# Kernel tuning notes

Measured on AMD Instinct MI355X. Metric: run time of the kernel, lower is better.

Reference implementation:

```python
import jax, jax.numpy as jnp
import numpy as np

B, N_H, N = 32, 16, 64
R, REP, NUM_CLS = 1024, 1024, 117
NUM_ITER = 2
T_LIS, K_LIS, W_LIS = 8.3, 12.0, 10.0

# static pair indices: x in [0,n_h), y in [0,n), x != y  -> M = N_H*N - N_H
_xx, _yy = np.meshgrid(np.arange(N_H), np.arange(N), indexing='ij')
_mask = _xx != _yy
X_IDX = jnp.asarray(_xx[_mask], dtype=jnp.int32)  # [M]
Y_IDX = jnp.asarray(_yy[_mask], dtype=jnp.int32)  # [M]
M = int(_mask.sum())


def lis(x):
    # low-grade suppression
    return T_LIS / (1.0 + jnp.exp(K_LIS - W_LIS * x))


def setup_inputs() -> dict:
    key = jax.random.key(0)
    ks = jax.random.split(key, 18)
    s = 0.02
    p = lambda k, shp: (jax.random.normal(k, shp) * s).astype(jnp.float32)
    box_features = jax.random.normal(ks[0], (B, N, R), dtype=jnp.float32)
    box_coords = jax.random.uniform(ks[1], (B, N, 4), dtype=jnp.float32)
    box_labels = jax.random.randint(ks[2], (B, N), 0, NUM_CLS).astype(jnp.int32)
    box_labels = box_labels.at[:, :N_H].set(0)  # first N_H are humans (human_idx=0)
    box_scores = jax.random.uniform(ks[3], (B, N), dtype=jnp.float32)
    return {
        'box_features': box_features, 'box_coords': box_coords,
        'box_labels': box_labels, 'box_scores': box_scores,
        'W1': p(ks[4], (2 * R, REP)), 'b1': jnp.zeros((REP,), jnp.float32),
        'W2': p(ks[5], (REP, REP // 2)), 'b2': jnp.zeros((REP // 2,), jnp.float32),
        'W3': p(ks[6], (REP // 2, 1)), 'b3': jnp.zeros((1,), jnp.float32),
        'Ws': p(ks[7], (R, REP)), 'bs': jnp.zeros((REP,), jnp.float32),
        'Wo': p(ks[8], (R, REP)), 'bo': jnp.zeros((REP,), jnp.float32),
        'Wsu': p(ks[9], (R + REP, R)),
        'Wou': p(ks[10], (R + REP, R)),
    }


def reference(box_features, box_coords, box_labels, box_scores,
              W1, b1, W2, b2, W3, b3, Ws, bs, Wo, bo, Wsu, Wou):
    def per_image(enc, coords, labels, scores):
        # enc: [N, R]
        A = jnp.zeros((N_H, N), enc.dtype)
        for _ in range(NUM_ITER):
            pe = jnp.concatenate([enc[X_IDX], enc[Y_IDX]], axis=1)  # [M, 2R]
            h = jax.nn.relu(pe @ W1 + b1)
            h = jax.nn.relu(h @ W2 + b2)
            w = (h @ W3 + b3)[:, 0]  # [M]
            A = jnp.zeros((N_H, N), enc.dtype).at[X_IDX, Y_IDX].set(jax.nn.sigmoid(w))
            msg_h = A @ jax.nn.relu(enc @ Wo + bo)                      # [N_H, REP]
            enc_h = jnp.concatenate([enc[:N_H], msg_h], axis=1) @ Wsu  # [N_H, R]
            enc = enc.at[:N_H].set(enc_h)
            msg_o = A.T @ jax.nn.relu(enc_h @ Ws + bs)                  # [N, REP]
            enc = jnp.concatenate([enc, msg_o], axis=1) @ Wou           # [N, R]
        pair = jnp.concatenate([enc[X_IDX], enc[Y_IDX]], axis=1)  # [M, 2R]
        prod = lis(scores[X_IDX]) * lis(scores[Y_IDX])            # [M]
        # identity object_class_to_target_class: class c -> [c]
        prior = jnp.zeros((M, NUM_CLS), enc.dtype).at[jnp.arange(M), labels[Y_IDX]].set(prod)
        prior = A[X_IDX, Y_IDX][:, None] * prior
        return pair, coords[X_IDX], coords[Y_IDX], prior

    pair, bh, bo_, prior = jax.vmap(per_image)(box_features, box_coords, box_labels, box_scores)
    return (pair.reshape(B * M, 2 * R), bh, bo_, prior.reshape(B * M, NUM_CLS))
```

## Files before the change

kernel.cpp:

```cpp
#include <hip/hip_runtime.h>

#define B_   32
#define N_   64
#define NH   16
#define R_   1024
#define REP  1024
#define M_   1008
#define BM   (B_ * M_)
#define NCLS 117

#define MD_DIRECT 0
#define MD_CC1    2
#define MD_CC2    3

typedef short bhalf8 __attribute__((ext_vector_type(8)));
typedef float f32x4  __attribute__((ext_vector_type(4)));

typedef __attribute__((address_space(3))) void       lds_t;
typedef const __attribute__((address_space(1))) void gbl_t;
__device__ __forceinline__ void gld16(const void* g, void* l)
{
    __builtin_amdgcn_global_load_lds((gbl_t*)g, (lds_t*)l, 16, 0, 0);
}

__device__ __forceinline__ unsigned short f2bf(float f)
{
    union { float f; unsigned int u; } x; x.f = f;
    unsigned int r = x.u + 0x7FFFu + ((x.u >> 16) & 1u);
    return (unsigned short)(r >> 16);
}
__device__ __forceinline__ float bf2f(unsigned short u)
{
    union { unsigned int i; float f; } x; x.i = ((unsigned int)u) << 16; return x.f;
}
__device__ __forceinline__ unsigned int addrelu2(unsigned int a, unsigned int b)
{
    float lo = fmaxf(bf2f((unsigned short)(a & 0xffff)) + bf2f((unsigned short)(b & 0xffff)), 0.f);
    float hi = fmaxf(bf2f((unsigned short)(a >> 16))    + bf2f((unsigned short)(b >> 16)),    0.f);
    return (unsigned int)f2bf(lo) | ((unsigned int)f2bf(hi) << 16);
}

__device__ __forceinline__ void tr32(const float* in, unsigned short* out,
                                     int K, int N, int local)
{
    __shared__ float t[32][33];
    int kb = K >> 5;
    int k0 = (local % kb) * 32, n0 = (local / kb) * 32;
    int tx = threadIdx.x & 31, ty = threadIdx.x >> 5;
#pragma unroll
    for (int r = 0; r < 4; ++r)
        t[ty + r * 8][tx] = in[(size_t)(k0 + ty + r * 8) * N + n0 + tx];
    __syncthreads();
#pragma unroll
    for (int r = 0; r < 4; ++r)
        out[(size_t)(n0 + ty + r * 8) * K + k0 + tx] = f2bf(t[tx][ty + r * 8]);
}

__global__ __launch_bounds__(256)
void prep_all(const float* __restrict__ W1, const float* __restrict__ W2,
              const float* __restrict__ Wo, const float* __restrict__ Ws,
              const float* __restrict__ Wsu, const float* __restrict__ Wou,
              const float* __restrict__ bo_, const float* __restrict__ b1_,
              unsigned short* __restrict__ Wfused, unsigned short* __restrict__ W2t,
              unsigned short* __restrict__ Wst, unsigned short* __restrict__ Wsut,
              unsigned short* __restrict__ Wout, float* __restrict__ biasFull)
{
    int bx = blockIdx.x;
    if      (bx < 1024) tr32(W1 + 1024 * 1024, Wfused,               1024, 1024, bx);
    else if (bx < 2048) tr32(Wo,               Wfused + 1024 * 1024, 1024, 1024, bx - 1024);
    else if (bx < 3072) tr32(W1,               Wfused + 2048 * 1024, 1024, 1024, bx - 2048);
    else if (bx < 3584) tr32(W2,  W2t,  1024, 512,  bx - 3072);
    else if (bx < 4608) tr32(Ws,  Wst,  1024, 1024, bx - 3584);
    else if (bx < 6656) tr32(Wsu, Wsut, 2048, 1024, bx - 4608);
    else if (bx < 8704) tr32(Wou, Wout, 2048, 1024, bx - 6656);
    else {
        int c = (bx - 8704) * 256 + threadIdx.x;
        float v = 0.f;
        if (c >= 2048)      v = b1_[c - 2048];
        else if (c >= 1024) v = bo_[c - 1024];
        biasFull[c] = v;
    }
}

__global__ void cvt_bf(const float* __restrict__ in, unsigned short* __restrict__ out)
{
    int i = blockIdx.x * 256 + threadIdx.x;
    float4 a = ((const float4*)in)[2 * i];
    float4 b = ((const float4*)in)[2 * i + 1];
    uint4 o;
    o.x = (unsigned)f2bf(a.x) | ((unsigned)f2bf(a.y) << 16);
    o.y = (unsigned)f2bf(a.z) | ((unsigned)f2bf(a.w) << 16);
    o.z = (unsigned)f2bf(b.x) | ((unsigned)f2bf(b.y) << 16);
    o.w = (unsigned)f2bf(b.z) | ((unsigned)f2bf(b.w) << 16);
    ((uint4*)out)[i] = o;
}

__global__ __launch_bounds__(256)
void gemm_uvgo(const unsigned short* __restrict__ enc,
               const unsigned short* __restrict__ Wf,
               const float* __restrict__ biasFull, unsigned short* __restrict__ XX)
{
    __shared__ unsigned short As[128 * 32];
    __shared__ unsigned short Bs[128 * 32];
    const int tid  = threadIdx.x;
    const int lane = tid & 63, wave = tid >> 6;
    const int wm = wave & 1, wn = wave >> 1;
    const int l15 = lane & 15, lk = lane >> 4;
    const int row0 = blockIdx.y * 128, col0 = blockIdx.x * 128;
    const int kq = (lane & 3) * 8;

    const unsigned short* pA[2];
    const unsigned short* pB[2];
    unsigned short* AsW[2];
    unsigned short* BsW[2];
#pragma unroll
    for (int i = 0; i < 2; ++i) {
        int tr = wave * 32 + (lane >> 2) + i * 16;
        pA[i]  = enc + (size_t)(row0 + tr) * 1024 + kq;
        pB[i]  = Wf  + (size_t)(col0 + tr) * 1024 + kq;
        AsW[i] = As + wave * 1024 + i * 512 + lane * 8;
        BsW[i] = Bs + wave * 1024 + i * 512 + lane * 8;
    }

    f32x4 acc[4][4];
#pragma unroll
    for (int i = 0; i < 4; ++i)
#pragma unroll
    for (int j = 0; j < 4; ++j) acc[i][j] = (f32x4)0.f;

    for (int k0 = 0; k0 < 1024; k0 += 32) {
        __syncthreads();
        gld16(pA[0] + k0, AsW[0]);
        gld16(pA[1] + k0, AsW[1]);
        gld16(pB[0] + k0, BsW[0]);
        gld16(pB[1] + k0, BsW[1]);
        __syncthreads();
        bhalf8 af[4], bf4[4];
#pragma unroll
        for (int mt = 0; mt < 4; ++mt)
            af[mt] = *(bhalf8*)&As[(wm * 64 + mt * 16 + l15) * 32 + lk * 8];
#pragma unroll
        for (int nt = 0; nt < 4; ++nt)
            bf4[nt] = *(bhalf8*)&Bs[(wn * 64 + nt * 16 + l15) * 32 + lk * 8];
#pragma unroll
        for (int mt = 0; mt < 4; ++mt)
#pragma unroll
        for (int nt = 0; nt < 4; ++nt)
            acc[mt][nt] = __builtin_amdgcn_mfma_f32_16x16x32_bf16(af[mt], bf4[nt],
                                                                  acc[mt][nt], 0, 0, 0);
    }

#pragma unroll
    for (int mt = 0; mt < 4; ++mt)
#pragma unroll
    for (int r = 0; r < 4; ++r) {
        int row = row0 + wm * 64 + mt * 16 + lk * 4 + r;
#pragma unroll
        for (int nt = 0; nt < 4; ++nt) {
            int col = col0 + wn * 64 + nt * 16 + l15;
            float v = acc[mt][nt][r] + biasFull[col];
            if ((col >> 10) == 1) v = fmaxf(v, 0.f);
            XX[(size_t)row * 3072 + col] = f2bf(v);
        }
    }
}

__global__ __launch_bounds__(256)
void pair_bf(const unsigned short* __restrict__ XX,
             const unsigned short* __restrict__ W2t, const float* __restrict__ b2,
             const float* __restrict__ W3f, float* __restrict__ wpart)
{
    __shared__ unsigned short As[128 * 32];
    __shared__ unsigned short Bs[128 * 32];
    __shared__ float red[2][128];
    const int tid  = threadIdx.x;
    const int lane = tid & 63, wave = tid >> 6;
    const int wm = wave & 1, wn = wave >> 1;
    const int l15 = lane & 15, lk = lane >> 4;
    const int row0 = blockIdx.y * 128, col0 = blockIdx.x * 128;

    const int srow = tid >> 1, skh = tid & 1;
    int rg = row0 + srow;
    int b  = rg / M_, m = rg % M_;
    int x  = m / 63, jj = m % 63;
    int y  = jj + (jj >= x ? 1 : 0);
    const unsigned short* Up = XX + ((size_t)(b * 64 + x)) * 3072 + 2048 + skh * 16;
    const unsigned short* Vp = XX + ((size_t)(b * 64 + y)) * 3072 + skh * 16;
    unsigned short* AsW = As + srow * 32 + skh * 16;

    const int kq = (lane & 3) * 8;
    const unsigned short* pB[2];
    unsigned short* BsW[2];
#pragma unroll
    for (int i = 0; i < 2; ++i) {
        int tr = wave * 32 + (lane >> 2) + i * 16;
        pB[i]  = W2t + (size_t)(col0 + tr) * REP + kq;
        BsW[i] = Bs + wave * 1024 + i * 512 + lane * 8;
    }

    f32x4 acc[4][4];
#pragma unroll
    for (int i = 0; i < 4; ++i)
#pragma unroll
    for (int j = 0; j < 4; ++j) acc[i][j] = (f32x4)0.f;

    for (int k0 = 0; k0 < REP; k0 += 32) {
        uint4 uu0 = *(const uint4*)(Up + k0);
        uint4 uu1 = *(const uint4*)(Up + k0 + 8);
        uint4 vv0 = *(const uint4*)(Vp + k0);
        uint4 vv1 = *(const uint4*)(Vp + k0 + 8);
        uint4 h0, h1;
        h0.x = addrelu2(uu0.x, vv0.x); h0.y = addrelu2(uu0.y, vv0.y);
        h0.z = addrelu2(uu0.z, vv0.z); h0.w = addrelu2(uu0.w, vv0.w);
        h1.x = addrelu2(uu1.x, vv1.x); h1.y = addrelu2(uu1.y, vv1.y);
        h1.z = addrelu2(uu1.z, vv1.z); h1.w = addrelu2(uu1.w, vv1.w);
        __syncthreads();
        *(uint4*)(AsW)     = h0;
        *(uint4*)(AsW + 8) = h1;
        gld16(pB[0] + k0, BsW[0]);
        gld16(pB[1] + k0, BsW[1]);
        __syncthreads();
        bhalf8 af[4], bf4[4];
#pragma unroll
        for (int mt = 0; mt < 4; ++mt)
            af[mt] = *(bhalf8*)&As[(wm * 64 + mt * 16 + l15) * 32 + lk * 8];
#pragma unroll
        for (int nt = 0; nt < 4; ++nt)
            bf4[nt] = *(bhalf8*)&Bs[(wn * 64 + nt * 16 + l15) * 32 + lk * 8];
#pragma unroll
        for (int mt = 0; mt < 4; ++mt)
#pragma unroll
        for (int nt = 0; nt < 4; ++nt)
            acc[mt][nt] = __builtin_amdgcn_mfma_f32_16x16x32_bf16(af[mt], bf4[nt],
                                                                  acc[mt][nt], 0, 0, 0);
    }

    float b2v[4], w3v[4];
#pragma unroll
    for (int nt = 0; nt < 4; ++nt) {
        int col = col0 + wn * 64 + nt * 16 + l15;
        b2v[nt] = b2[col];
        w3v[nt] = W3f[col];
    }
#pragma unroll
    for (int mt = 0; mt < 4; ++mt)
#pragma unroll
    for (int r = 0; r < 4; ++r) {
        int rloc = wm * 64 + mt * 16 + lk * 4 + r;
        float p = 0.f;
#pragma unroll
        for (int nt = 0; nt < 4; ++nt)
            p += fmaxf(acc[mt][nt][r] + b2v[nt], 0.f) * w3v[nt];
        p += __shfl_xor(p, 1); p += __shfl_xor(p, 2);
        p += __shfl_xor(p, 4); p += __shfl_xor(p, 8);
        if (l15 == 0) red[wn][rloc] = p;
    }
    __syncthreads();
    if (tid < 128)
        wpart[blockIdx.x * BM + row0 + tid] = red[0][tid] + red[1][tid];
}

__device__ __forceinline__ void compute_A(const float* __restrict__ wpart, float b3v,
                                          int b, float* Al, int t)
{
    for (int i = t; i < NH * N_; i += 128) {
        int y = i & 63, x = i >> 6;
        float v = 0.f;
        if (y != x) {
            int j = y - (y > x ? 1 : 0);
            int r = b * M_ + x * 63 + j;
            float s = b3v + wpart[r] + wpart[BM + r] + wpart[2 * BM + r] + wpart[3 * BM + r];
            v = 1.f / (1.f + expf(-s));
        }
        Al[i] = v;
    }
}

__global__ __launch_bounds__(128)
void msgh_kernel(const float* __restrict__ wpart, const float* __restrict__ b3,
                 const unsigned short* __restrict__ XX,
                 unsigned short* __restrict__ msgh, float* __restrict__ Aw)
{
    __shared__ float Al[NH * N_];
    __shared__ float Gl[N_][128];
    int b = blockIdx.x, c0 = blockIdx.y * 128, t = threadIdx.x;
    compute_A(wpart, b3[0], b, Al, t);
    for (int y = 0; y < N_; ++y)
        Gl[y][t] = bf2f(XX[((size_t)(b * 64 + y)) * 3072 + 1024 + c0 + t]);
    __syncthreads();
    if (blockIdx.y == 0)
        for (int i = t; i < NH * N_; i += 128) Aw[b * NH * N_ + i] = Al[i];
    for (int x = 0; x < NH; ++x) {
        float s = 0.f;
#pragma unroll 8
        for (int y = 0; y < N_; ++y) s += Al[x * N_ + y] * Gl[y][t];
        msgh[((size_t)(b * NH + x)) * REP + c0 + t] = f2bf(s);
    }
}

__global__ __launch_bounds__(128)
void msgo_kernel(const float* __restrict__ wpart, const float* __restrict__ b3,
                 const unsigned short* __restrict__ Gs, unsigned short* __restrict__ msgo)
{
    __shared__ float Al[NH * N_];
    __shared__ float Gl[NH][128];
    int b = blockIdx.x, c0 = blockIdx.y * 128, t = threadIdx.x;
    compute_A(wpart, b3[0], b, Al, t);
    for (int x = 0; x < NH; ++x)
        Gl[x][t] = bf2f(Gs[((size_t)(b * NH + x)) * REP + c0 + t]);
    __syncthreads();
    for (int y = 0; y < N_; ++y) {
        float s = 0.f;
#pragma unroll
        for (int x = 0; x < NH; ++x) s += Al[x * N_ + y] * Gl[x][t];
        msgo[((size_t)(b * N_ + y)) * REP + c0 + t] = f2bf(s);
    }
}

__global__ __launch_bounds__(256)
void gemm_small(const unsigned short* __restrict__ A1, const unsigned short* __restrict__ A2,
                const unsigned short* __restrict__ A3, const unsigned short* __restrict__ Bt,
                const float* __restrict__ bias, float* __restrict__ Cf,
                unsigned short* __restrict__ Cb, int K, int Nc, int doRelu, int mode)
{
    __shared__ unsigned short As[64 * 32];
    __shared__ unsigned short Bs[64 * 32];
    const int tid  = threadIdx.x;
    const int lane = tid & 63, wave = tid >> 6;
    const int wr = wave & 1, wc = wave >> 1;
    const int l15 = lane & 15, lk = lane >> 4;
    const int row0 = blockIdx.y * 64, col0 = blockIdx.x * 64;
    const int kq = (lane & 3) * 8;

    int tr = wave * 16 + (lane >> 2);
    int rr = row0 + tr;
    const unsigned short* p1;
    const unsigned short* p2 = nullptr;
    if (mode == MD_DIRECT) {
        p1 = A1 + (size_t)rr * K;
    } else if (mode == MD_CC1) {
        int b = rr >> 4, x = rr & 15;
        p1 = A1 + (size_t)(b * 64 + x) * 1024;
        p2 = A2 + (size_t)rr * 1024 - 1024;
    } else {
        int b = rr >> 6, n = rr & 63;
        p1 = (n < 16) ? A3 + (size_t)(b * 16 + n) * 1024
                      : A1 + (size_t)rr * 1024;
        p2 = A2 + (size_t)rr * 1024 - 1024;
    }
    const unsigned short* pA1 = p1 + kq;
    const unsigned short* pA2 = p2 ? p2 + kq : nullptr;
    const unsigned short* pB  = Bt + (size_t)(col0 + tr) * K + kq;
    unsigned short* AsW = As + wave * 512 + lane * 8;
    unsigned short* BsW = Bs + wave * 512 + lane * 8;
    const int kSw = (mode != MD_DIRECT) ? 1024 : K;

    f32x4 acc[2][2];
#pragma unroll
    for (int i = 0; i < 2; ++i)
#pragma unroll
    for (int j = 0; j < 2; ++j) acc[i][j] = (f32x4)0.f;

    for (int k0 = 0; k0 < K; k0 += 32) {
        const unsigned short* a = (k0 < kSw) ? pA1 : pA2;
        __syncthreads();
        gld16(a + k0,  AsW);
        gld16(pB + k0, BsW);
        __syncthreads();
        bhalf8 af[2], bf4[2];
#pragma unroll
        for (int mt = 0; mt < 2; ++mt)
            af[mt] = *(bhalf8*)&As[(wr * 32 + mt * 16 + l15) * 32 + lk * 8];
#pragma unroll
        for (int nt = 0; nt < 2; ++nt)
            bf4[nt] = *(bhalf8*)&Bs[(wc * 32 + nt * 16 + l15) * 32 + lk * 8];
#pragma unroll
        for (int mt = 0; mt < 2; ++mt)
#pragma unroll
        for (int nt = 0; nt < 2; ++nt)
            acc[mt][nt] = __builtin_amdgcn_mfma_f32_16x16x32_bf16(af[mt], bf4[nt],
                                                                  acc[mt][nt], 0, 0, 0);
    }

#pragma unroll
    for (int mt = 0; mt < 2; ++mt)
#pragma unroll
    for (int r = 0; r < 4; ++r) {
        int row = row0 + wr * 32 + mt * 16 + lk * 4 + r;
#pragma unroll
        for (int nt = 0; nt < 2; ++nt) {
            int col = col0 + wc * 32 + nt * 16 + l15;
            float v = acc[mt][nt][r];
            if (bias) v += bias[col];
            if (doRelu) v = fmaxf(v, 0.f);
            if (Cf) Cf[(size_t)row * Nc + col] = v;
            if (Cb) Cb[(size_t)row * Nc + col] = f2bf(v);
        }
    }
}

__global__ void pair_out(const float* __restrict__ enc, float* __restrict__ out0)
{
    int i = blockIdx.x * 256 + threadIdx.x;
    if (i >= BM * 512) return;
    int r = i >> 9, q = i & 511;
    int b = r / M_, m = r % M_;
    int x = m / 63, j = m % 63;
    int y = j + (j >= x ? 1 : 0);
    const float4* e4 = (const float4*)enc;
    float4 v = (q < 256) ? e4[(b * 64 + x) * 256 + q]
                         : e4[(b * 64 + y) * 256 + (q - 256)];
    ((float4*)out0)[i] = v;
}

__global__ void coords_out(const float* __restrict__ coords,
                           float* __restrict__ out1, float* __restrict__ out2)
{
    int r = blockIdx.x * 256 + threadIdx.x;
    if (r >= BM) return;
    int b = r / M_, m = r % M_;
    int x = m / 63, j = m % 63;
    int y = j + (j >= x ? 1 : 0);
    const float4* c4 = (const float4*)coords;
    ((float4*)out1)[r] = c4[b * 64 + x];
    ((float4*)out2)[r] = c4[b * 64 + y];
}

__device__ __forceinline__ float lis_f(float x)
{
    return 8.3f / (1.f + expf(12.f - 10.f * x));
}

__global__ void prior_out(const float* __restrict__ Aw, const int* __restrict__ labels,
                          const float* __restrict__ scores, float* __restrict__ out3)
{
    int i = blockIdx.x * 256 + threadIdx.x;
    if (i >= BM * NCLS) return;
    int r = i / NCLS, c = i % NCLS;
    int b = r / M_, m = r % M_;
    int x = m / 63, j = m % 63;
    int y = j + (j >= x ? 1 : 0);
    int lab = labels[b * 64 + y];
    float val = 0.f;
    if (c == lab) {
        float sx = scores[b * 64 + x], sy = scores[b * 64 + y];
        val = Aw[(b * NH + x) * N_ + y] * lis_f(sx) * lis_f(sy);
    }
    out3[i] = val;
}

extern "C" void kernel_launch(void* const* d_in, const int* in_sizes, int n_in,
                              void* d_out, int out_size, void* d_ws, size_t ws_size,
                              hipStream_t stream)
{
    const float* box_features = (const float*)d_in[0];
    const float* box_coords   = (const float*)d_in[1];
    const int*   box_labels   = (const int*)d_in[2];
    const float* box_scores   = (const float*)d_in[3];
    const float* W1  = (const float*)d_in[4];
    const float* b1  = (const float*)d_in[5];
    const float* W2  = (const float*)d_in[6];
    const float* b2  = (const float*)d_in[7];
    const float* W3  = (const float*)d_in[8];
    const float* b3  = (const float*)d_in[9];
    const float* Ws  = (const float*)d_in[10];
    const float* bs  = (const float*)d_in[11];
    const float* Wo  = (const float*)d_in[12];
    const float* bo  = (const float*)d_in[13];
    const float* Wsu = (const float*)d_in[14];
    const float* Wou = (const float*)d_in[15];

    float* wsf  = (float*)d_ws;
    float* encA = wsf;           wsf += (size_t)B_ * N_ * R_;
    float* wpart= wsf;           wsf += (size_t)4 * BM;
    float* Aw   = wsf;           wsf += (size_t)B_ * NH * N_;
    float* biasFull = wsf;       wsf += 3072;

    unsigned short* wsu = (unsigned short*)wsf;
    unsigned short* enc0bf = wsu;  wsu += (size_t)B_ * N_ * R_;
    unsigned short* encIbf = wsu;  wsu += (size_t)B_ * N_ * R_;
    unsigned short* XX     = wsu;  wsu += (size_t)B_ * N_ * 3072;
    unsigned short* msghbf = wsu;  wsu += (size_t)B_ * NH * REP;
    unsigned short* enchbf = wsu;  wsu += (size_t)B_ * NH * R_;
    unsigned short* Gsbf   = wsu;  wsu += (size_t)B_ * NH * REP;
    unsigned short* msgobf = wsu;  wsu += (size_t)B_ * N_ * REP;
    unsigned short* Wfused = wsu;  wsu += (size_t)3072 * 1024;
    unsigned short* W2t    = wsu;  wsu += (size_t)512 * 1024;
    unsigned short* Wst    = wsu;  wsu += (size_t)1024 * 1024;
    unsigned short* Wsut   = wsu;  wsu += (size_t)1024 * 2048;
    unsigned short* Wout   = wsu;  wsu += (size_t)1024 * 2048;

    float* out0 = (float*)d_out;
    float* out1 = out0 + (size_t)BM * 2048;
    float* out2 = out1 + (size_t)BM * 4;
    float* out3 = out2 + (size_t)BM * 4;

    prep_all<<<8716, 256, 0, stream>>>(W1, W2, Wo, Ws, Wsu, Wou, bo, b1,
                                       Wfused, W2t, Wst, Wsut, Wout, biasFull);
    cvt_bf<<<1024, 256, 0, stream>>>(box_features, enc0bf);

    for (int it = 0; it < 2; ++it) {
        const unsigned short* enc = (it == 0) ? enc0bf : encIbf;
        gemm_uvgo<<<dim3(24, 16), 256, 0, stream>>>(enc, Wfused, biasFull, XX);
        pair_bf<<<dim3(4, 252), 256, 0, stream>>>(XX, W2t, b2, W3, wpart);
        msgh_kernel<<<dim3(32, 8), 128, 0, stream>>>(wpart, b3, XX, msghbf, Aw);
        gemm_small<<<dim3(16, 8), 256, 0, stream>>>(enc, msghbf, nullptr, Wsut, nullptr,
                                                    nullptr, enchbf, 2048, 1024, 0, MD_CC1);
        gemm_small<<<dim3(16, 8), 256, 0, stream>>>(enchbf, nullptr, nullptr, Wst, bs,
                                                    nullptr, Gsbf, 1024, 1024, 1, MD_DIRECT);
        msgo_kernel<<<dim3(32, 8), 128, 0, stream>>>(wpart, b3, Gsbf, msgobf);
        gemm_small<<<dim3(16, 32), 256, 0, stream>>>(enc, msgobf, enchbf, Wout, nullptr,
                                                     (it == 1) ? encA : nullptr,
                                                     (it == 0) ? encIbf : nullptr,
                                                     1024 * 2, 1024, 0, MD_CC2);
    }

    pair_out<<<64512, 256, 0, stream>>>(encA, out0);
    coords_out<<<126, 256, 0, stream>>>(box_coords, out1, out2);
    prior_out<<<14742, 256, 0, stream>>>(Aw, box_labels, box_scores, out3);
}
```

Baseline: 761.2 us.

## Multi-buffer LDS pipelines in GEMMs and merge output and prep launches

The three GEMM kernels now keep several LDS slots of async global-to-LDS loads in flight: three slots in gemm_uvgo and pair_bf, four in gemm_small. Each stage waits with explicit vmcnt/lgkmcnt counts and a single barrier pair, instead of syncing around every tile load. pair_bf also prefetches its next U/V rows into registers, and addrelu2 uses a packed bf16 convert instruction. The bf16 input conversion is folded into prep_all and the three output kernels into one launch, which removes launch gaps. The hand-written waitcnt values depend on the exact number of outstanding loads and are fragile, and the extra LDS may lower occupancy.

After: 751.5 us. About the same (-1.3%).

```diff
diff --git a/kernel.cpp b/kernel.cpp
--- a/kernel.cpp
+++ b/kernel.cpp
@@ -33,11 +33,32 @@
 {
     union { unsigned int i; float f; } x; x.i = ((unsigned int)u) << 16; return x.f;
 }
+
 __device__ __forceinline__ unsigned int addrelu2(unsigned int a, unsigned int b)
 {
-    float lo = fmaxf(bf2f((unsigned short)(a & 0xffff)) + bf2f((unsigned short)(b & 0xffff)), 0.f);
-    float hi = fmaxf(bf2f((unsigned short)(a >> 16))    + bf2f((unsigned short)(b >> 16)),    0.f);
-    return (unsigned int)f2bf(lo) | ((unsigned int)f2bf(hi) << 16);
+    union { unsigned int u; float f; } la, ha, lb, hb;
+    la.u = a << 16;          ha.u = a & 0xffff0000u;
+    lb.u = b << 16;          hb.u = b & 0xffff0000u;
+    float lo = fmaxf(la.f + lb.f, 0.f);
+    float hi = fmaxf(ha.f + hb.f, 0.f);
+    unsigned int r;
+    asm("v_cvt_pk_bf16_f32 %0, %1, %2" : "=v"(r) : "v"(lo), "v"(hi));
+    return r;
+}
+
+__device__ __forceinline__ void wait_vm(int n)
+{
+    if (n >= 8)      asm volatile("s_waitcnt vmcnt(8)" ::: "memory");
+    else if (n == 6) asm volatile("s_waitcnt vmcnt(6)" ::: "memory");
+    else if (n == 4) asm volatile("s_waitcnt vmcnt(4)" ::: "memory");
+    else if (n == 2) asm volatile("s_waitcnt vmcnt(2)" ::: "memory");
+    else             asm volatile("s_waitcnt vmcnt(0)" ::: "memory");
+}
+__device__ __forceinline__ void wait_vm_lgkm(int n)
+{
+    if (n >= 12)      asm volatile("s_waitcnt vmcnt(12) lgkmcnt(0)" ::: "memory");
+    else if (n >= 10) asm volatile("s_waitcnt vmcnt(10) lgkmcnt(0)" ::: "memory");
+    else              asm volatile("s_waitcnt vmcnt(8) lgkmcnt(0)" ::: "memory");
 }
 
 __device__ __forceinline__ void tr32(const float* in, unsigned short* out,
@@ -61,9 +82,11 @@
               const float* __restrict__ Wo, const float* __restrict__ Ws,
               const float* __restrict__ Wsu, const float* __restrict__ Wou,
               const float* __restrict__ bo_, const float* __restrict__ b1_,
+              const float* __restrict__ feat,
               unsigned short* __restrict__ Wfused, unsigned short* __restrict__ W2t,
               unsigned short* __restrict__ Wst, unsigned short* __restrict__ Wsut,
-              unsigned short* __restrict__ Wout, float* __restrict__ biasFull)
+              unsigned short* __restrict__ Wout, float* __restrict__ biasFull,
+              unsigned short* __restrict__ enc0bf)
 {
     int bx = blockIdx.x;
     if      (bx < 1024) tr32(W1 + 1024 * 1024, Wfused,               1024, 1024, bx);
@@ -73,26 +96,23 @@
     else if (bx < 4608) tr32(Ws,  Wst,  1024, 1024, bx - 3584);
     else if (bx < 6656) tr32(Wsu, Wsut, 2048, 1024, bx - 4608);
     else if (bx < 8704) tr32(Wou, Wout, 2048, 1024, bx - 6656);
-    else {
+    else if (bx < 8716) {
         int c = (bx - 8704) * 256 + threadIdx.x;
         float v = 0.f;
         if (c >= 2048)      v = b1_[c - 2048];
         else if (c >= 1024) v = bo_[c - 1024];
         biasFull[c] = v;
-    }
-}
-
-__global__ void cvt_bf(const float* __restrict__ in, unsigned short* __restrict__ out)
-{
-    int i = blockIdx.x * 256 + threadIdx.x;
-    float4 a = ((const float4*)in)[2 * i];
-    float4 b = ((const float4*)in)[2 * i + 1];
-    uint4 o;
-    o.x = (unsigned)f2bf(a.x) | ((unsigned)f2bf(a.y) << 16);
-    o.y = (unsigned)f2bf(a.z) | ((unsigned)f2bf(a.w) << 16);
-    o.z = (unsigned)f2bf(b.x) | ((unsigned)f2bf(b.y) << 16);
-    o.w = (unsigned)f2bf(b.z) | ((unsigned)f2bf(b.w) << 16);
-    ((uint4*)out)[i] = o;
+    } else {
+        int i = (bx - 8716) * 256 + threadIdx.x;
+        float4 a = ((const float4*)feat)[2 * i];
+        float4 b = ((const float4*)feat)[2 * i + 1];
+        uint4 o;
+        o.x = (unsigned)f2bf(a.x) | ((unsigned)f2bf(a.y) << 16);
+        o.y = (unsigned)f2bf(a.z) | ((unsigned)f2bf(a.w) << 16);
+        o.z = (unsigned)f2bf(b.x) | ((unsigned)f2bf(b.y) << 16);
+        o.w = (unsigned)f2bf(b.z) | ((unsigned)f2bf(b.w) << 16);
+        ((uint4*)enc0bf)[i] = o;
+    }
 }
 
 __global__ __launch_bounds__(256)
@@ -100,8 +120,8 @@
                const unsigned short* __restrict__ Wf,
                const float* __restrict__ biasFull, unsigned short* __restrict__ XX)
 {
-    __shared__ unsigned short As[128 * 32];
-    __shared__ unsigned short Bs[128 * 32];
+    __shared__ unsigned short As[3][128 * 32];
+    __shared__ unsigned short Bs[3][128 * 32];
     const int tid  = threadIdx.x;
     const int lane = tid & 63, wave = tid >> 6;
     const int wm = wave & 1, wn = wave >> 1;
@@ -111,16 +131,20 @@
 
     const unsigned short* pA[2];
     const unsigned short* pB[2];
-    unsigned short* AsW[2];
-    unsigned short* BsW[2];
+    int ldsOff[2];
 #pragma unroll
     for (int i = 0; i < 2; ++i) {
         int tr = wave * 32 + (lane >> 2) + i * 16;
         pA[i]  = enc + (size_t)(row0 + tr) * 1024 + kq;
         pB[i]  = Wf  + (size_t)(col0 + tr) * 1024 + kq;
-        AsW[i] = As + wave * 1024 + i * 512 + lane * 8;
-        BsW[i] = Bs + wave * 1024 + i * 512 + lane * 8;
-    }
+        ldsOff[i] = wave * 1024 + i * 512 + lane * 8;
+    }
+
+#define STG_UV(slot, k0) do {                          \
+        gld16(pA[0] + (k0), &As[slot][ldsOff[0]]);     \
+        gld16(pA[1] + (k0), &As[slot][ldsOff[1]]);     \
+        gld16(pB[0] + (k0), &Bs[slot][ldsOff[0]]);     \
+        gld16(pB[1] + (k0), &Bs[slot][ldsOff[1]]); } while (0)
 
     f32x4 acc[4][4];
 #pragma unroll
@@ -128,27 +152,31 @@
 #pragma unroll
     for (int j = 0; j < 4; ++j) acc[i][j] = (f32x4)0.f;
 
-    for (int k0 = 0; k0 < 1024; k0 += 32) {
-        __syncthreads();
-        gld16(pA[0] + k0, AsW[0]);
-        gld16(pA[1] + k0, AsW[1]);
-        gld16(pB[0] + k0, BsW[0]);
-        gld16(pB[1] + k0, BsW[1]);
-        __syncthreads();
+    STG_UV(0, 0);
+    STG_UV(1, 32);
+    for (int t = 0; t < 32; ++t) {
+        const int slot = t % 3;
+        if (t + 2 < 32) STG_UV((t + 2) % 3, (t + 2) * 32);
+        wait_vm(t < 30 ? 8 : (t == 30 ? 4 : 0));
+        __builtin_amdgcn_s_barrier();
+        __builtin_amdgcn_sched_barrier(0);
         bhalf8 af[4], bf4[4];
 #pragma unroll
         for (int mt = 0; mt < 4; ++mt)
-            af[mt] = *(bhalf8*)&As[(wm * 64 + mt * 16 + l15) * 32 + lk * 8];
+            af[mt] = *(bhalf8*)&As[slot][(wm * 64 + mt * 16 + l15) * 32 + lk * 8];
 #pragma unroll
         for (int nt = 0; nt < 4; ++nt)
-            bf4[nt] = *(bhalf8*)&Bs[(wn * 64 + nt * 16 + l15) * 32 + lk * 8];
+            bf4[nt] = *(bhalf8*)&Bs[slot][(wn * 64 + nt * 16 + l15) * 32 + lk * 8];
 #pragma unroll
         for (int mt = 0; mt < 4; ++mt)
 #pragma unroll
         for (int nt = 0; nt < 4; ++nt)
             acc[mt][nt] = __builtin_amdgcn_mfma_f32_16x16x32_bf16(af[mt], bf4[nt],
                                                                   acc[mt][nt], 0, 0, 0);
-    }
+        __builtin_amdgcn_sched_barrier(0);
+        __builtin_amdgcn_s_barrier();
+    }
+#undef STG_UV
 
 #pragma unroll
     for (int mt = 0; mt < 4; ++mt)
@@ -171,7 +199,7 @@
              const float* __restrict__ W3f, float* __restrict__ wpart)
 {
     __shared__ unsigned short As[128 * 32];
-    __shared__ unsigned short Bs[128 * 32];
+    __shared__ unsigned short Bs[3][128 * 32];
     __shared__ float red[2][128];
     const int tid  = threadIdx.x;
     const int lane = tid & 63, wave = tid >> 6;
@@ -190,13 +218,17 @@
 
     const int kq = (lane & 3) * 8;
     const unsigned short* pB[2];
-    unsigned short* BsW[2];
+    int bO[2];
 #pragma unroll
     for (int i = 0; i < 2; ++i) {
         int tr = wave * 32 + (lane >> 2) + i * 16;
-        pB[i]  = W2t + (size_t)(col0 + tr) * REP + kq;
-        BsW[i] = Bs + wave * 1024 + i * 512 + lane * 8;
-    }
+        pB[i] = W2t + (size_t)(col0 + tr) * REP + kq;
+        bO[i] = wave * 1024 + i * 512 + lane * 8;
+    }
+
+#define STG_B(slot, k0) do {                        \
+        gld16(pB[0] + (k0), &Bs[slot][bO[0]]);      \
+        gld16(pB[1] + (k0), &Bs[slot][bO[1]]); } while (0)
 
     f32x4 acc[4][4];
 #pragma unroll
@@ -204,36 +236,51 @@
 #pragma unroll
     for (int j = 0; j < 4; ++j) acc[i][j] = (f32x4)0.f;
 
-    for (int k0 = 0; k0 < REP; k0 += 32) {
-        uint4 uu0 = *(const uint4*)(Up + k0);
-        uint4 uu1 = *(const uint4*)(Up + k0 + 8);
-        uint4 vv0 = *(const uint4*)(Vp + k0);
-        uint4 vv1 = *(const uint4*)(Vp + k0 + 8);
+    uint4 cu0 = *(const uint4*)(Up);
+    uint4 cu1 = *(const uint4*)(Up + 8);
+    uint4 cv0 = *(const uint4*)(Vp);
+    uint4 cv1 = *(const uint4*)(Vp + 8);
+    STG_B(0, 0);
+    STG_B(1, 32);
+
+    for (int t = 0; t < 32; ++t) {
+        const int slot = t % 3;
+        const int kn = (t + 1 < 32) ? (t + 1) * 32 : 0;
+        uint4 nu0 = *(const uint4*)(Up + kn);
+        uint4 nu1 = *(const uint4*)(Up + kn + 8);
+        uint4 nv0 = *(const uint4*)(Vp + kn);
+        uint4 nv1 = *(const uint4*)(Vp + kn + 8);
+        if (t + 2 < 32) STG_B((t + 2) % 3, (t + 2) * 32);
+
         uint4 h0, h1;
-        h0.x = addrelu2(uu0.x, vv0.x); h0.y = addrelu2(uu0.y, vv0.y);
-        h0.z = addrelu2(uu0.z, vv0.z); h0.w = addrelu2(uu0.w, vv0.w);
-        h1.x = addrelu2(uu1.x, vv1.x); h1.y = addrelu2(uu1.y, vv1.y);
-        h1.z = addrelu2(uu1.z, vv1.z); h1.w = addrelu2(uu1.w, vv1.w);
-        __syncthreads();
+        h0.x = addrelu2(cu0.x, cv0.x); h0.y = addrelu2(cu0.y, cv0.y);
+        h0.z = addrelu2(cu0.z, cv0.z); h0.w = addrelu2(cu0.w, cv0.w);
+        h1.x = addrelu2(cu1.x, cv1.x); h1.y = addrelu2(cu1.y, cv1.y);
+        h1.z = addrelu2(cu1.z, cv1.z); h1.w = addrelu2(cu1.w, cv1.w);
         *(uint4*)(AsW)     = h0;
         *(uint4*)(AsW + 8) = h1;
-        gld16(pB[0] + k0, BsW[0]);
-        gld16(pB[1] + k0, BsW[1]);
-        __syncthreads();
+
+        wait_vm_lgkm(t == 0 ? 8 : (t < 30 ? 12 : (t == 30 ? 10 : 8)));
+        __builtin_amdgcn_s_barrier();
+        __builtin_amdgcn_sched_barrier(0);
         bhalf8 af[4], bf4[4];
 #pragma unroll
         for (int mt = 0; mt < 4; ++mt)
             af[mt] = *(bhalf8*)&As[(wm * 64 + mt * 16 + l15) * 32 + lk * 8];
 #pragma unroll
         for (int nt = 0; nt < 4; ++nt)
-            bf4[nt] = *(bhalf8*)&Bs[(wn * 64 + nt * 16 + l15) * 32 + lk * 8];
+            bf4[nt] = *(bhalf8*)&Bs[slot][(wn * 64 + nt * 16 + l15) * 32 + lk * 8];
 #pragma unroll
         for (int mt = 0; mt < 4; ++mt)
 #pragma unroll
         for (int nt = 0; nt < 4; ++nt)
             acc[mt][nt] = __builtin_amdgcn_mfma_f32_16x16x32_bf16(af[mt], bf4[nt],
                                                                   acc[mt][nt], 0, 0, 0);
-    }
+        __builtin_amdgcn_sched_barrier(0);
+        __builtin_amdgcn_s_barrier();
+        cu0 = nu0; cu1 = nu1; cv0 = nv0; cv1 = nv1;
+    }
+#undef STG_B
 
     float b2v[4], w3v[4];
 #pragma unroll
@@ -323,8 +370,8 @@
                 const float* __restrict__ bias, float* __restrict__ Cf,
                 unsigned short* __restrict__ Cb, int K, int Nc, int doRelu, int mode)
 {
-    __shared__ unsigned short As[64 * 32];
-    __shared__ unsigned short Bs[64 * 32];
+    __shared__ unsigned short As[4][64 * 32];
+    __shared__ unsigned short Bs[4][64 * 32];
     const int tid  = threadIdx.x;
     const int lane = tid & 63, wave = tid >> 6;
     const int wr = wave & 1, wc = wave >> 1;
@@ -351,9 +398,14 @@
     const unsigned short* pA1 = p1 + kq;
     const unsigned short* pA2 = p2 ? p2 + kq : nullptr;
     const unsigned short* pB  = Bt + (size_t)(col0 + tr) * K + kq;
-    unsigned short* AsW = As + wave * 512 + lane * 8;
-    unsigned short* BsW = Bs + wave * 512 + lane * 8;
+    const int stO = wave * 512 + lane * 8;
     const int kSw = (mode != MD_DIRECT) ? 1024 : K;
+    const int NT = K >> 5;
+
+#define STG_MID(slot, k0) do {                                  \
+        const unsigned short* ap = ((k0) < kSw) ? pA1 : pA2;    \
+        gld16(ap + (k0), &As[slot][stO]);                       \
+        gld16(pB + (k0), &Bs[slot][stO]); } while (0)
 
     f32x4 acc[2][2];
 #pragma unroll
@@ -361,26 +413,33 @@
 #pragma unroll
     for (int j = 0; j < 2; ++j) acc[i][j] = (f32x4)0.f;
 
-    for (int k0 = 0; k0 < K; k0 += 32) {
-        const unsigned short* a = (k0 < kSw) ? pA1 : pA2;
-        __syncthreads();
-        gld16(a + k0,  AsW);
-        gld16(pB + k0, BsW);
-        __syncthreads();
+    STG_MID(0, 0);
+    STG_MID(1, 32);
+    STG_MID(2, 64);
+    for (int t = 0; t < NT; ++t) {
+        const int slot = t & 3;
+        if (t + 3 < NT) STG_MID((t + 3) & 3, (t + 3) * 32);
+        int rem = NT - 1 - t;
+        wait_vm(rem >= 3 ? 6 : rem * 2);
+        __builtin_amdgcn_s_barrier();
+        __builtin_amdgcn_sched_barrier(0);
         bhalf8 af[2], bf4[2];
 #pragma unroll
         for (int mt = 0; mt < 2; ++mt)
-            af[mt] = *(bhalf8*)&As[(wr * 32 + mt * 16 + l15) * 32 + lk * 8];
+            af[mt] = *(bhalf8*)&As[slot][(wr * 32 + mt * 16 + l15) * 32 + lk * 8];
 #pragma unroll
         for (int nt = 0; nt < 2; ++nt)
-            bf4[nt] = *(bhalf8*)&Bs[(wc * 32 + nt * 16 + l15) * 32 + lk * 8];
+            bf4[nt] = *(bhalf8*)&Bs[slot][(wc * 32 + nt * 16 + l15) * 32 + lk * 8];
 #pragma unroll
         for (int mt = 0; mt < 2; ++mt)
 #pragma unroll
         for (int nt = 0; nt < 2; ++nt)
             acc[mt][nt] = __builtin_amdgcn_mfma_f32_16x16x32_bf16(af[mt], bf4[nt],
                                                                   acc[mt][nt], 0, 0, 0);
-    }
+        __builtin_amdgcn_sched_barrier(0);
+        __builtin_amdgcn_s_barrier();
+    }
+#undef STG_MID
 
 #pragma unroll
     for (int mt = 0; mt < 2; ++mt)
@@ -399,54 +458,51 @@
     }
 }
 
-__global__ void pair_out(const float* __restrict__ enc, float* __restrict__ out0)
-{
-    int i = blockIdx.x * 256 + threadIdx.x;
-    if (i >= BM * 512) return;
-    int r = i >> 9, q = i & 511;
-    int b = r / M_, m = r % M_;
-    int x = m / 63, j = m % 63;
-    int y = j + (j >= x ? 1 : 0);
-    const float4* e4 = (const float4*)enc;
-    float4 v = (q < 256) ? e4[(b * 64 + x) * 256 + q]
-                         : e4[(b * 64 + y) * 256 + (q - 256)];
-    ((float4*)out0)[i] = v;
-}
-
-__global__ void coords_out(const float* __restrict__ coords,
-                           float* __restrict__ out1, float* __restrict__ out2)
-{
-    int r = blockIdx.x * 256 + threadIdx.x;
-    if (r >= BM) return;
-    int b = r / M_, m = r % M_;
-    int x = m / 63, j = m % 63;
-    int y = j + (j >= x ? 1 : 0);
-    const float4* c4 = (const float4*)coords;
-    ((float4*)out1)[r] = c4[b * 64 + x];
-    ((float4*)out2)[r] = c4[b * 64 + y];
-}
-
 __device__ __forceinline__ float lis_f(float x)
 {
     return 8.3f / (1.f + expf(12.f - 10.f * x));
 }
 
-__global__ void prior_out(const float* __restrict__ Aw, const int* __restrict__ labels,
-                          const float* __restrict__ scores, float* __restrict__ out3)
-{
-    int i = blockIdx.x * 256 + threadIdx.x;
-    if (i >= BM * NCLS) return;
-    int r = i / NCLS, c = i % NCLS;
-    int b = r / M_, m = r % M_;
-    int x = m / 63, j = m % 63;
-    int y = j + (j >= x ? 1 : 0);
-    int lab = labels[b * 64 + y];
-    float val = 0.f;
-    if (c == lab) {
-        float sx = scores[b * 64 + x], sy = scores[b * 64 + y];
-        val = Aw[(b * NH + x) * N_ + y] * lis_f(sx) * lis_f(sy);
-    }
-    out3[i] = val;
+__global__ __launch_bounds__(256)
+void outputs_all(const float* __restrict__ enc, const float* __restrict__ coords,
+                 const float* __restrict__ Aw, const int* __restrict__ labels,
+                 const float* __restrict__ scores,
+                 float* __restrict__ out0, float* __restrict__ out1,
+                 float* __restrict__ out2, float* __restrict__ out3)
+{
+    int bx = blockIdx.x;
+    if (bx < 64512) {
+        int i = bx * 256 + threadIdx.x;
+        int r = i >> 9, q = i & 511;
+        int b = r / M_, m = r % M_;
+        int x = m / 63, j = m % 63;
+        int y = j + (j >= x ? 1 : 0);
+        const float4* e4 = (const float4*)enc;
+        float4 v = (q < 256) ? e4[(b * 64 + x) * 256 + q]
+                             : e4[(b * 64 + y) * 256 + (q - 256)];
+        ((float4*)out0)[i] = v;
+    } else if (bx < 64638) {
+        int r = (bx - 64512) * 256 + threadIdx.x;
+        int b = r / M_, m = r % M_;
+        int x = m / 63, j = m % 63;
+        int y = j + (j >= x ? 1 : 0);
+        const float4* c4 = (const float4*)coords;
+        ((float4*)out1)[r] = c4[b * 64 + x];
+        ((float4*)out2)[r] = c4[b * 64 + y];
+    } else {
+        int i = (bx - 64638) * 256 + threadIdx.x;
+        int r = i / NCLS, c = i % NCLS;
+        int b = r / M_, m = r % M_;
+        int x = m / 63, j = m % 63;
+        int y = j + (j >= x ? 1 : 0);
+        int lab = labels[b * 64 + y];
+        float val = 0.f;
+        if (c == lab) {
+            float sx = scores[b * 64 + x], sy = scores[b * 64 + y];
+            val = Aw[(b * NH + x) * N_ + y] * lis_f(sx) * lis_f(sy);
+        }
+        out3[i] = val;
+    }
 }
 
 extern "C" void kernel_launch(void* const* d_in, const int* in_sizes, int n_in,
@@ -495,9 +551,8 @@
     float* out2 = out1 + (size_t)BM * 4;
     float* out3 = out2 + (size_t)BM * 4;
 
-    prep_all<<<8716, 256, 0, stream>>>(W1, W2, Wo, Ws, Wsu, Wou, bo, b1,
-                                       Wfused, W2t, Wst, Wsut, Wout, biasFull);
-    cvt_bf<<<1024, 256, 0, stream>>>(box_features, enc0bf);
+    prep_all<<<9740, 256, 0, stream>>>(W1, W2, Wo, Ws, Wsu, Wou, bo, b1, box_features,
+                                       Wfused, W2t, Wst, Wsut, Wout, biasFull, enc0bf);
 
     for (int it = 0; it < 2; ++it) {
         const unsigned short* enc = (it == 0) ? enc0bf : encIbf;
@@ -515,7 +570,6 @@
                                                      1024 * 2, 1024, 0, MD_CC2);
     }
 
-    pair_out<<<64512, 256, 0, stream>>>(encA, out0);
-    coords_out<<<126, 256, 0, stream>>>(box_coords, out1, out2);
-    prior_out<<<14742, 256, 0, stream>>>(Aw, box_labels, box_scores, out3);
-}
+    outputs_all<<<79380, 256, 0, stream>>>(encA, box_coords, Aw, box_labels, box_scores,
+                                           out0, out1, out2, out3);
+}
```
